# Kernel tuning notes

Hardware: AMD Instinct MI355X
Metric: run time of the kernel (lower is better)

Reference implementation:

```python
import jax, jax.numpy as jnp
import numpy as np

B, T, D, H = 2, 2048, 1024, 16
DH = D // H

def setup_inputs() -> dict:
    key = jax.random.key(0)
    ks = jax.random.split(key, 5)
    scale = 1.0 / np.sqrt(D)
    x = jax.random.normal(ks[0], (B, T, D), dtype=jnp.float32)
    Wq = jax.random.normal(ks[1], (D, D), dtype=jnp.float32) * scale
    Wk = jax.random.normal(ks[2], (D, D), dtype=jnp.float32) * scale
    Wv = jax.random.normal(ks[3], (D, D), dtype=jnp.float32) * scale
    Wo = jax.random.normal(ks[4], (D, D), dtype=jnp.float32) * scale
    # causal mask: True means masked (matches torch masked_fill semantics)
    mask = jnp.triu(jnp.ones((T, T), dtype=bool), k=1)
    return {"x": x, "mask": mask, "Wq": Wq, "Wk": Wk, "Wv": Wv, "Wo": Wo}

def reference(x, mask, Wq, Wk, Wv, Wo):
    b, t, c = x.shape
    # projections -> [B, H, T, DH]
    def split_heads(y):
        return y.reshape(b, t, H, DH).transpose(0, 2, 1, 3)
    q = split_heads(x @ Wq)
    k = split_heads(x @ Wk)
    v = split_heads(x @ Wv)
    # scores [B, H, T, T]
    att = jnp.einsum('bhqd,bhkd->bhqk', q, k) / jnp.sqrt(jnp.float32(DH))
    att = jnp.where(mask, -jnp.inf, att)
    att = jax.nn.softmax(att, axis=-1)
    # dropout=0.0 (eval-mode determinism)
    out = jnp.einsum('bhqk,bhkd->bhqd', att, v)
    out = out.transpose(0, 2, 1, 3).reshape(b, t, c)
    return out @ Wo
```

## Files before the change

kernel.cpp:

```cpp
#include <hip/hip_runtime.h>
#include <stdint.h>

typedef unsigned short u16;
typedef unsigned int u32;
typedef __attribute__((ext_vector_type(8))) short s16x8;
typedef __attribute__((ext_vector_type(4))) float f32x4;
typedef __attribute__((ext_vector_type(8))) unsigned short u16x8;
typedef __attribute__((ext_vector_type(4))) unsigned short u16x4;

#define T_ 2048
#define D_ 1024
#define H_ 16
#define DH_ 64

#define QSCALE_LOG2E 0.18033688011112042f

#if __has_builtin(__builtin_amdgcn_exp2f)
#define EXP2(x) __builtin_amdgcn_exp2f(x)
#else
#define EXP2(x) exp2f(x)
#endif

__device__ __forceinline__ float bf2f(u16 u) {
    union { unsigned int i; float f; } x; x.i = ((unsigned int)u) << 16; return x.f;
}
__device__ __forceinline__ u16 f2bf(float f) {
    union { float f; unsigned int i; } x; x.f = f;
    unsigned int u = x.i;
    u += 0x7fffu + ((u >> 16) & 1u);
    return (u16)(u >> 16);
}
__device__ __forceinline__ u32 pack_rn(float a, float b) {
    union { float f; u32 u; } ua, ub; ua.f = a; ub.f = b;
    return ((ua.u + 0x8000u) >> 16) | ((ub.u + 0x8000u) & 0xffff0000u);
}
__device__ __forceinline__ u32 cvtpk(float lo, float hi) {
    u32 r;
    asm("v_cvt_pk_bf16_f32 %0, %1, %2" : "=v"(r) : "v"(lo), "v"(hi));
    return r;
}
__device__ __forceinline__ void plswap32(u32 &a, u32 &b) {
    asm("v_permlane32_swap_b32 %0, %1" : "+v"(a), "+v"(b));
}
__device__ __forceinline__ void plswap16(u32 &a, u32 &b) {
    asm("v_permlane16_swap_b32 %0, %1" : "+v"(a), "+v"(b));
}
__device__ __forceinline__ s16x8 frag4(u32 a, u32 b, u32 c, u32 d) {
    union { u32 u[4]; s16x8 v; } x;
    x.u[0] = a; x.u[1] = b; x.u[2] = c; x.u[3] = d; return x.v;
}
__device__ __forceinline__ void p_frags(const f32x4 s[4], s16x8 &p0, s16x8 &p1) {
    u32 w00 = cvtpk(s[0][0], s[0][1]), w01 = cvtpk(s[0][2], s[0][3]);
    u32 w10 = cvtpk(s[1][0], s[1][1]), w11 = cvtpk(s[1][2], s[1][3]);
    u32 w20 = cvtpk(s[2][0], s[2][1]), w21 = cvtpk(s[2][2], s[2][3]);
    u32 w30 = cvtpk(s[3][0], s[3][1]), w31 = cvtpk(s[3][2], s[3][3]);
    plswap32(w00, w10); plswap16(w00, w10);
    plswap32(w01, w11); plswap16(w01, w11);
    plswap32(w20, w30); plswap16(w20, w30);
    plswap32(w21, w31); plswap16(w21, w31);
    p0 = frag4(w00, w01, w10, w11);
    p1 = frag4(w20, w21, w30, w31);
}

__device__ __forceinline__ void gload16(const u16* g, u16* l) {
    __builtin_amdgcn_global_load_lds(
        (const __attribute__((address_space(1))) void*)g,
        (__attribute__((address_space(3))) void*)l,
        16, 0, 0);
}

__global__ __launch_bounds__(256) void prep_kernel(const float* __restrict__ x,
                                                   const float* __restrict__ Wq,
                                                   const float* __restrict__ Wk,
                                                   const float* __restrict__ Wv,
                                                   const float* __restrict__ Wo,
                                                   u16* __restrict__ xb,
                                                   u16* __restrict__ WT) {
    __shared__ float tile[32][33];
    int blk = blockIdx.x;
    if (blk < 4096) {
        int i = (blk * 256 + threadIdx.x) * 4;
        float4 v = *(const float4*)(x + i);
        u16x4 o;
        o[0] = f2bf(v.x); o[1] = f2bf(v.y); o[2] = f2bf(v.z); o[3] = f2bf(v.w);
        *(u16x4*)(xb + i) = o;
    } else {
        int t = blk - 4096;
        int s = t >> 10;
        const float* W = (s == 0) ? Wq : (s == 1) ? Wk : (s == 2) ? Wv : Wo;
        int n0 = ((t >> 5) & 31) * 32;
        int k0 = (t & 31) * 32;
        int tx = threadIdx.x & 31, ty = threadIdx.x >> 5;
        #pragma unroll
        for (int j = 0; j < 32; j += 8)
            tile[ty + j][tx] = W[(k0 + ty + j) * D_ + n0 + tx];
        __syncthreads();
        u16* dst = WT + (size_t)s * D_ * D_;
        int row = threadIdx.x >> 3;
        int cg  = (threadIdx.x & 7) << 2;
        u16x4 o;
        #pragma unroll
        for (int j = 0; j < 4; ++j) o[j] = f2bf(tile[cg + j][row]);
        *(u16x4*)(dst + (size_t)(n0 + row) * D_ + k0 + cg) = o;
    }
}

__global__ __launch_bounds__(256) void gemm_qkv(const u16* __restrict__ A,
                                                const u16* __restrict__ Bt,
                                                u16* __restrict__ Qw,
                                                u16* __restrict__ Kw,
                                                u16* __restrict__ Vw) {
    __shared__ __align__(16) u16 As[2][128 * 32];
    __shared__ __align__(16) u16 Bs[2][128 * 32];
    const int m0 = blockIdx.x * 128, n0 = blockIdx.y * 128;
    int tid = threadIdx.x;
    int w = tid >> 6, lane = tid & 63, quad = lane >> 4, l15 = lane & 15;
    int wr = w >> 1, wc = w & 1;

    int nb0 = (w << 7), nb1 = nb0 + 64;
    int c0 = nb0 + lane, c1 = nb1 + lane;
    int r0 = c0 >> 2, k0off = (((c0 & 3) ^ ((r0 >> 1) & 3)) << 3);
    int r1 = c1 >> 2, k1off = (((c1 & 3) ^ ((r1 >> 1) & 3)) << 3);
    const u16* Ar0 = A + (size_t)(m0 + r0) * D_ + k0off;
    const u16* Ar1 = A + (size_t)(m0 + r1) * D_ + k1off;
    const u16* Br0 = Bt + (size_t)(n0 + r0) * D_ + k0off;
    const u16* Br1 = Bt + (size_t)(n0 + r1) * D_ + k1off;

    f32x4 acc[4][4];
    #pragma unroll
    for (int mi = 0; mi < 4; ++mi)
        #pragma unroll
        for (int ni = 0; ni < 4; ++ni) acc[mi][ni] = (f32x4){0.f, 0.f, 0.f, 0.f};

    gload16(Ar0, &As[0][nb0 << 3]);
    gload16(Ar1, &As[0][nb1 << 3]);
    gload16(Br0, &Bs[0][nb0 << 3]);
    gload16(Br1, &Bs[0][nb1 << 3]);

    for (int k0 = 0; k0 < D_; k0 += 32) {
        int buf = (k0 >> 5) & 1;
        __syncthreads();
        if (k0 + 32 < D_) {
            int kn = k0 + 32;
            gload16(Ar0 + kn, &As[buf ^ 1][nb0 << 3]);
            gload16(Ar1 + kn, &As[buf ^ 1][nb1 << 3]);
            gload16(Br0 + kn, &Bs[buf ^ 1][nb0 << 3]);
            gload16(Br1 + kn, &Bs[buf ^ 1][nb1 << 3]);
        }
        s16x8 af[4], bf[4];
        #pragma unroll
        for (int mi = 0; mi < 4; ++mi) {
            int R = wr * 64 + mi * 16 + l15;
            af[mi] = *(const s16x8*)&As[buf][((R << 2) | (quad ^ ((R >> 1) & 3))) << 3];
        }
        #pragma unroll
        for (int ni = 0; ni < 4; ++ni) {
            int R = wc * 64 + ni * 16 + l15;
            bf[ni] = *(const s16x8*)&Bs[buf][((R << 2) | (quad ^ ((R >> 1) & 3))) << 3];
        }
        #pragma unroll
        for (int mi = 0; mi < 4; ++mi)
            #pragma unroll
            for (int ni = 0; ni < 4; ++ni)
                acc[mi][ni] = __builtin_amdgcn_mfma_f32_16x16x32_bf16(af[mi], bf[ni],
                                                                      acc[mi][ni], 0, 0, 0);
    }

    #pragma unroll
    for (int mi = 0; mi < 4; ++mi) {
        int mbase = m0 + wr * 64 + mi * 16 + quad * 4;
        #pragma unroll
        for (int ni = 0; ni < 4; ++ni) {
            int n = n0 + wc * 64 + ni * 16 + l15;
            int b = mbase >> 11, t0 = mbase & 2047;
            int sel = n >> 10, nn = n & 1023;
            int h = nn >> 6, dh = nn & 63;
            int bhidx = (b << 4) + h;
            if (sel == 0) {
                #pragma unroll
                for (int r = 0; r < 4; ++r)
                    Qw[(size_t)(bhidx * T_ + t0 + r) * DH_ + dh] =
                        f2bf(acc[mi][ni][r] * QSCALE_LOG2E);
            } else if (sel == 1) {
                #pragma unroll
                for (int r = 0; r < 4; ++r)
                    Kw[(size_t)(bhidx * T_ + t0 + r) * DH_ + dh] = f2bf(acc[mi][ni][r]);
            } else {
                uint2 pk;
                pk.x = pack_rn(acc[mi][ni][0], acc[mi][ni][1]);
                pk.y = pack_rn(acc[mi][ni][2], acc[mi][ni][3]);
                *(uint2*)(Vw + ((size_t)bhidx * DH_ + dh) * T_ + t0) = pk;
            }
        }
    }
}

__global__ __launch_bounds__(256) void gemm_out(const u16* __restrict__ A,
                                                const u16* __restrict__ Bt,
                                                float* __restrict__ Cout) {
    __shared__ __align__(16) u16 As[2][128 * 32];
    __shared__ __align__(16) u16 Bs[2][128 * 32];
    const int m0 = blockIdx.x * 128, n0 = blockIdx.y * 128;
    int tid = threadIdx.x;
    int w = tid >> 6, lane = tid & 63, quad = lane >> 4, l15 = lane & 15;
    int wr = w >> 1, wc = w & 1;

    int nb0 = (w << 7), nb1 = nb0 + 64;
    int c0 = nb0 + lane, c1 = nb1 + lane;
    int r0 = c0 >> 2, k0off = (((c0 & 3) ^ ((r0 >> 1) & 3)) << 3);
    int r1 = c1 >> 2, k1off = (((c1 & 3) ^ ((r1 >> 1) & 3)) << 3);
    const u16* Ar0 = A + (size_t)(m0 + r0) * D_ + k0off;
    const u16* Ar1 = A + (size_t)(m0 + r1) * D_ + k1off;
    const u16* Br0 = Bt + (size_t)(n0 + r0) * D_ + k0off;
    const u16* Br1 = Bt + (size_t)(n0 + r1) * D_ + k1off;

    f32x4 acc[4][4];
    #pragma unroll
    for (int mi = 0; mi < 4; ++mi)
        #pragma unroll
        for (int ni = 0; ni < 4; ++ni) acc[mi][ni] = (f32x4){0.f, 0.f, 0.f, 0.f};

    gload16(Ar0, &As[0][nb0 << 3]);
    gload16(Ar1, &As[0][nb1 << 3]);
    gload16(Br0, &Bs[0][nb0 << 3]);
    gload16(Br1, &Bs[0][nb1 << 3]);

    for (int k0 = 0; k0 < D_; k0 += 32) {
        int buf = (k0 >> 5) & 1;
        __syncthreads();
        if (k0 + 32 < D_) {
            int kn = k0 + 32;
            gload16(Ar0 + kn, &As[buf ^ 1][nb0 << 3]);
            gload16(Ar1 + kn, &As[buf ^ 1][nb1 << 3]);
            gload16(Br0 + kn, &Bs[buf ^ 1][nb0 << 3]);
            gload16(Br1 + kn, &Bs[buf ^ 1][nb1 << 3]);
        }
        s16x8 af[4], bf[4];
        #pragma unroll
        for (int mi = 0; mi < 4; ++mi) {
            int R = wr * 64 + mi * 16 + l15;
            af[mi] = *(const s16x8*)&As[buf][((R << 2) | (quad ^ ((R >> 1) & 3))) << 3];
        }
        #pragma unroll
        for (int ni = 0; ni < 4; ++ni) {
            int R = wc * 64 + ni * 16 + l15;
            bf[ni] = *(const s16x8*)&Bs[buf][((R << 2) | (quad ^ ((R >> 1) & 3))) << 3];
        }
        #pragma unroll
        for (int mi = 0; mi < 4; ++mi)
            #pragma unroll
            for (int ni = 0; ni < 4; ++ni)
                acc[mi][ni] = __builtin_amdgcn_mfma_f32_16x16x32_bf16(af[mi], bf[ni],
                                                                      acc[mi][ni], 0, 0, 0);
    }

    #pragma unroll
    for (int mi = 0; mi < 4; ++mi) {
        int mbase = m0 + wr * 64 + mi * 16 + quad * 4;
        #pragma unroll
        for (int ni = 0; ni < 4; ++ni) {
            int n = n0 + wc * 64 + ni * 16 + l15;
            #pragma unroll
            for (int r = 0; r < 4; ++r)
                Cout[(size_t)(mbase + r) * D_ + n] = acc[mi][ni][r];
        }
    }
}

__global__ __launch_bounds__(256, 4) void attn_mfma_kernel(const u16* __restrict__ Qg,
                                                           const u16* __restrict__ Kg,
                                                           const u16* __restrict__ Vt,
                                                           u16* __restrict__ Opart,
                                                           float* __restrict__ lpart) {
    __shared__ __align__(16) u16 Kbuf[2][64 * 64];
    __shared__ __align__(16) u16 Vbuf[2][64 * 64];

    int blk = blockIdx.x;
    int xcd = blk & 7, slot = blk >> 3;
    int bh = (xcd << 2) + (slot / 40);
    int x  = slot % 40;
    int BX, c;
    if (x < 4)       { BX = x;                    c = 0; }
    else if (x < 12) { BX = 4 + ((x - 4) >> 1);   c = (x - 4) & 1; }
    else if (x < 24) { BX = 8 + (x - 12) / 3;     c = (x - 12) % 3; }
    else             { BX = 12 + ((x - 24) >> 2); c = (x - 24) & 3; }
    int ktm = 2 * BX + 1;
    int ntile = ktm + 1;
    int nch = (BX >> 2) + 1;
    int base = ntile / nch, rem = ntile % nch;
    int kstart = c * base + (c < rem ? c : rem);
    int kend = kstart + base + (c < rem ? 1 : 0);

    int tid = threadIdx.x;
    int w = tid >> 6, lane = tid & 63, quad = lane >> 4, l15 = lane & 15;
    int q0 = BX << 7;
    int qA = q0 + 16 * w;
    int qB = q0 + 64 + 16 * w;

    const u16* Qb = Qg + (size_t)bh * T_ * DH_;
    const u16* Kb = Kg + (size_t)bh * T_ * DH_;
    const u16* Vb = Vt + (size_t)bh * DH_ * T_;

    s16x8 qa0 = *(const s16x8*)(Qb + (size_t)(qA + l15) * DH_ + quad * 8);
    s16x8 qa1 = *(const s16x8*)(Qb + (size_t)(qA + l15) * DH_ + quad * 8 + 32);
    s16x8 qc0 = *(const s16x8*)(Qb + (size_t)(qB + l15) * DH_ + quad * 8);
    s16x8 qc1 = *(const s16x8*)(Qb + (size_t)(qB + l15) * DH_ + quad * 8 + 32);

    const s16x8 ones = frag4(0x3F803F80u, 0x3F803F80u, 0x3F803F80u, 0x3F803F80u);

    int nb0 = (w << 7), nb1 = nb0 + 64;
    int n0c = nb0 + lane, n1c = nb1 + lane;
    int r0 = n0c >> 3, c0s = n0c & 7, g0 = (r0 << 3) + (c0s ^ (r0 & 7));
    int r1 = n1c >> 3, c1s = n1c & 7, g1 = (r1 << 3) + (c1s ^ (r1 & 7));

    {
        int kb0 = kstart << 6;
        const u16* Ktile = Kb + (size_t)kb0 * DH_;
        gload16(Ktile + (g0 << 3), &Kbuf[0][nb0 << 3]);
        gload16(Ktile + (g1 << 3), &Kbuf[0][nb1 << 3]);
        gload16(Vb + (size_t)r0 * T_ + kb0 + ((g0 & 7) << 3), &Vbuf[0][nb0 << 3]);
        gload16(Vb + (size_t)r1 * T_ + kb0 + ((g1 & 7) << 3), &Vbuf[0][nb1 << 3]);
    }

    f32x4 oA[4] = {{0.f,0.f,0.f,0.f},{0.f,0.f,0.f,0.f},{0.f,0.f,0.f,0.f},{0.f,0.f,0.f,0.f}};
    f32x4 oB[4] = {{0.f,0.f,0.f,0.f},{0.f,0.f,0.f,0.f},{0.f,0.f,0.f,0.f},{0.f,0.f,0.f,0.f}};
    f32x4 oLA = {0.f, 0.f, 0.f, 0.f};
    f32x4 oLB = {0.f, 0.f, 0.f, 0.f};

    for (int kt = kstart; kt < kend; ++kt) {
        int buf = (kt - kstart) & 1;
        __syncthreads();

        if (kt + 1 < kend) {
            int kb2 = (kt + 1) << 6;
            const u16* Ktile = Kb + (size_t)kb2 * DH_;
            gload16(Ktile + (g0 << 3), &Kbuf[buf ^ 1][nb0 << 3]);
            gload16(Ktile + (g1 << 3), &Kbuf[buf ^ 1][nb1 << 3]);
            gload16(Vb + (size_t)r0 * T_ + kb2 + ((g0 & 7) << 3), &Vbuf[buf ^ 1][nb0 << 3]);
            gload16(Vb + (size_t)r1 * T_ + kb2 + ((g1 & 7) << 3), &Vbuf[buf ^ 1][nb1 << 3]);
        }

        const bool liveA = (kt < ktm);

        f32x4 sA[4], sB[4];
        #pragma unroll
        for (int g = 0; g < 4; ++g) {
            int r = (g << 4) + l15;
            int cc = quad ^ (r & 7);
            s16x8 ka0 = *(const s16x8*)&Kbuf[buf][((r << 3) + cc) << 3];
            s16x8 ka1 = *(const s16x8*)&Kbuf[buf][((r << 3) + (cc ^ 4)) << 3];
            f32x4 z = {0.f, 0.f, 0.f, 0.f};
            sB[g] = __builtin_amdgcn_mfma_f32_16x16x32_bf16(ka0, qc0, z, 0, 0, 0);
            sB[g] = __builtin_amdgcn_mfma_f32_16x16x32_bf16(ka1, qc1, sB[g], 0, 0, 0);
            if (liveA) {
                sA[g] = __builtin_amdgcn_mfma_f32_16x16x32_bf16(ka0, qa0, z, 0, 0, 0);
                sA[g] = __builtin_amdgcn_mfma_f32_16x16x32_bf16(ka1, qa1, sA[g], 0, 0, 0);
            }
        }

        if (liveA && kt == ktm - 1) {
            int rA = 16 * w + l15;
            #pragma unroll
            for (int g = 0; g < 4; ++g)
                #pragma unroll
                for (int r = 0; r < 4; ++r)
                    if ((g << 4) + (quad << 2) + r > rA) sA[g][r] = -INFINITY;
        }
        if (kt == ktm) {
            int rB = 16 * w + l15;
            #pragma unroll
            for (int g = 0; g < 4; ++g)
                #pragma unroll
                for (int r = 0; r < 4; ++r)
                    if ((g << 4) + (quad << 2) + r > rB) sB[g][r] = -INFINITY;
        }

        #pragma unroll
        for (int g = 0; g < 4; ++g) {
            sB[g][0] = EXP2(sB[g][0]);
            sB[g][1] = EXP2(sB[g][1]);
            sB[g][2] = EXP2(sB[g][2]);
            sB[g][3] = EXP2(sB[g][3]);
        }
        if (liveA) {
            #pragma unroll
            for (int g = 0; g < 4; ++g) {
                sA[g][0] = EXP2(sA[g][0]);
                sA[g][1] = EXP2(sA[g][1]);
                sA[g][2] = EXP2(sA[g][2]);
                sA[g][3] = EXP2(sA[g][3]);
            }
        }

        s16x8 pa0, pa1, pc0, pc1;
        p_frags(sB, pc0, pc1);
        if (liveA) p_frags(sA, pa0, pa1);

        oLB = __builtin_amdgcn_mfma_f32_16x16x32_bf16(ones, pc0, oLB, 0, 0, 0);
        oLB = __builtin_amdgcn_mfma_f32_16x16x32_bf16(ones, pc1, oLB, 0, 0, 0);
        if (liveA) {
            oLA = __builtin_amdgcn_mfma_f32_16x16x32_bf16(ones, pa0, oLA, 0, 0, 0);
            oLA = __builtin_amdgcn_mfma_f32_16x16x32_bf16(ones, pa1, oLA, 0, 0, 0);
        }

        #pragma unroll
        for (int g = 0; g < 4; ++g) {
            int r = (g << 4) + l15;
            int cc = quad ^ (r & 7);
            s16x8 va0 = *(const s16x8*)&Vbuf[buf][((r << 3) + cc) << 3];
            s16x8 va1 = *(const s16x8*)&Vbuf[buf][((r << 3) + (cc ^ 4)) << 3];
            oB[g] = __builtin_amdgcn_mfma_f32_16x16x32_bf16(va0, pc0, oB[g], 0, 0, 0);
            oB[g] = __builtin_amdgcn_mfma_f32_16x16x32_bf16(va1, pc1, oB[g], 0, 0, 0);
            if (liveA) {
                oA[g] = __builtin_amdgcn_mfma_f32_16x16x32_bf16(va0, pa0, oA[g], 0, 0, 0);
                oA[g] = __builtin_amdgcn_mfma_f32_16x16x32_bf16(va1, pa1, oA[g], 0, 0, 0);
            }
        }
    }

    int slotid = ((bh << 4) + BX) * 4 + c;
    u16* dA = Opart + ((size_t)slotid * 128 + 16 * w + l15) * 64;
    u16* dB = dA + 64 * 64;
    #pragma unroll
    for (int g = 0; g < 4; ++g) {
        uint2 pk;
        pk.x = cvtpk(oA[g][0], oA[g][1]); pk.y = cvtpk(oA[g][2], oA[g][3]);
        *(uint2*)(dA + (g << 4) + (quad << 2)) = pk;
        pk.x = cvtpk(oB[g][0], oB[g][1]); pk.y = cvtpk(oB[g][2], oB[g][3]);
        *(uint2*)(dB + (g << 4) + (quad << 2)) = pk;
    }
    if (quad == 0) {
        lpart[(size_t)slotid * 128 + 16 * w + l15] = oLA[0];
        lpart[(size_t)slotid * 128 + 64 + 16 * w + l15] = oLB[0];
    }
}

__global__ __launch_bounds__(256) void reduce_attn(const u16* __restrict__ Opart,
                                                   const float* __restrict__ lpart,
                                                   u16* __restrict__ att) {
    int BX = blockIdx.x, bh = blockIdx.y;
    int nch = (BX >> 2) + 1;
    int tid = threadIdx.x;
    int row = tid >> 1, dh0 = (tid & 1) << 5;
    int slotbase = ((bh << 4) + BX) << 2;

    float acc[32];
    #pragma unroll
    for (int i = 0; i < 32; ++i) acc[i] = 0.f;
    float l = 0.f;
    for (int cc = 0; cc < nch; ++cc) {
        const u16* op = Opart + ((size_t)(slotbase + cc) * 128 + row) * 64 + dh0;
        #pragma unroll
        for (int v = 0; v < 4; ++v) {
            u16x8 o8 = *(const u16x8*)(op + v * 8);
            #pragma unroll
            for (int j = 0; j < 8; ++j) acc[v * 8 + j] += bf2f(o8[j]);
        }
        l += lpart[(size_t)(slotbase + cc) * 128 + row];
    }
    float inv = 1.f / l;
    int b = bh >> 4, h = bh & 15;
    int q = (BX << 7) + row;
    u16* dst = att + ((size_t)(b * T_) + q) * D_ + (h << 6) + dh0;
    #pragma unroll
    for (int v = 0; v < 4; ++v) {
        u16x8 o8;
        #pragma unroll
        for (int j = 0; j < 8; ++j) o8[j] = f2bf(acc[v * 8 + j] * inv);
        *(u16x8*)(dst + v * 8) = o8;
    }
}

extern "C" void kernel_launch(void* const* d_in, const int* in_sizes, int n_in,
                              void* d_out, int out_size, void* d_ws, size_t ws_size,
                              hipStream_t stream) {
    const float* x  = (const float*)d_in[0];
    const float* Wq = (const float*)d_in[2];
    const float* Wk = (const float*)d_in[3];
    const float* Wv = (const float*)d_in[4];
    const float* Wo = (const float*)d_in[5];
    float* out = (float*)d_out;

    char* ws = (char*)d_ws;
    u16*   xb    = (u16*)(ws);
    u16*   WT    = (u16*)(ws + (8ull  << 20));
    u16*   Qw    = (u16*)(ws + (16ull << 20));
    u16*   Kw    = (u16*)(ws + (24ull << 20));
    u16*   Vw    = (u16*)(ws + (32ull << 20));
    u16*   att   = (u16*)(ws + (40ull << 20));
    u16*   Opart = (u16*)(ws + (48ull << 20));
    float* lpart = (float*)(ws + (82ull << 20));

    prep_kernel<<<dim3(8192), dim3(256), 0, stream>>>(x, Wq, Wk, Wv, Wo, xb, WT);
    gemm_qkv<<<dim3(32, 24), dim3(256), 0, stream>>>(xb, WT, Qw, Kw, Vw);
    attn_mfma_kernel<<<dim3(1280), dim3(256), 0, stream>>>(Qw, Kw, Vw, Opart, lpart);
    reduce_attn<<<dim3(16, 32), dim3(256), 0, stream>>>(Opart, lpart, att);
    gemm_out<<<dim3(32, 8), dim3(256), 0, stream>>>(att, WT + 3ull * 1048576ull, out);
}
```

Measured before the change: 186.3 us.

## Write unsplit attention tiles directly and halve output GEMM tile width

Attention tiles that run as a single KV chunk (nch==1) now normalise by the row sum and write bf16 output straight into the attention buffer. This skips the partial-buffer round trip, and reduce_attn now launches only for the split tiles (BX>=4). Separately, gemm_out switches from 128x128 to 128x64 tiles, doubling the grid to 512 blocks to improve CU occupancy on the small output GEMM, at the cost of more redundant A-tile loads.

```diff
diff --git a/kernel.cpp b/kernel.cpp
--- a/kernel.cpp
+++ b/kernel.cpp
@@ -199,55 +199,52 @@
                                                 const u16* __restrict__ Bt,
                                                 float* __restrict__ Cout) {
     __shared__ __align__(16) u16 As[2][128 * 32];
-    __shared__ __align__(16) u16 Bs[2][128 * 32];
-    const int m0 = blockIdx.x * 128, n0 = blockIdx.y * 128;
+    __shared__ __align__(16) u16 Bs[2][64 * 32];
+    const int m0 = blockIdx.x * 128, n0 = blockIdx.y * 64;
     int tid = threadIdx.x;
     int w = tid >> 6, lane = tid & 63, quad = lane >> 4, l15 = lane & 15;
-    int wr = w >> 1, wc = w & 1;
-
-    int nb0 = (w << 7), nb1 = nb0 + 64;
-    int c0 = nb0 + lane, c1 = nb1 + lane;
-    int r0 = c0 >> 2, k0off = (((c0 & 3) ^ ((r0 >> 1) & 3)) << 3);
-    int r1 = c1 >> 2, k1off = (((c1 & 3) ^ ((r1 >> 1) & 3)) << 3);
-    const u16* Ar0 = A + (size_t)(m0 + r0) * D_ + k0off;
-    const u16* Ar1 = A + (size_t)(m0 + r1) * D_ + k1off;
-    const u16* Br0 = Bt + (size_t)(n0 + r0) * D_ + k0off;
-    const u16* Br1 = Bt + (size_t)(n0 + r1) * D_ + k1off;
-
-    f32x4 acc[4][4];
+
+    int nbA0 = (w << 7), nbA1 = nbA0 + 64, nbB = (w << 6);
+    int cA0 = nbA0 + lane, cA1 = nbA1 + lane, cB = nbB + lane;
+    int rA0 = cA0 >> 2, kA0 = (((cA0 & 3) ^ ((rA0 >> 1) & 3)) << 3);
+    int rA1 = cA1 >> 2, kA1 = (((cA1 & 3) ^ ((rA1 >> 1) & 3)) << 3);
+    int rB  = cB >> 2,  kB  = (((cB  & 3) ^ ((rB  >> 1) & 3)) << 3);
+    const u16* ArA0 = A + (size_t)(m0 + rA0) * D_ + kA0;
+    const u16* ArA1 = A + (size_t)(m0 + rA1) * D_ + kA1;
+    const u16* BrB  = Bt + (size_t)(n0 + rB) * D_ + kB;
+
+    f32x4 acc[2][4];
     #pragma unroll
-    for (int mi = 0; mi < 4; ++mi)
+    for (int mi = 0; mi < 2; ++mi)
         #pragma unroll
         for (int ni = 0; ni < 4; ++ni) acc[mi][ni] = (f32x4){0.f, 0.f, 0.f, 0.f};
 
-    gload16(Ar0, &As[0][nb0 << 3]);
-    gload16(Ar1, &As[0][nb1 << 3]);
-    gload16(Br0, &Bs[0][nb0 << 3]);
-    gload16(Br1, &Bs[0][nb1 << 3]);
+    gload16(ArA0, &As[0][nbA0 << 3]);
+    gload16(ArA1, &As[0][nbA1 << 3]);
+    gload16(BrB,  &Bs[0][nbB << 3]);
 
     for (int k0 = 0; k0 < D_; k0 += 32) {
         int buf = (k0 >> 5) & 1;
         __syncthreads();
         if (k0 + 32 < D_) {
             int kn = k0 + 32;
-            gload16(Ar0 + kn, &As[buf ^ 1][nb0 << 3]);
-            gload16(Ar1 + kn, &As[buf ^ 1][nb1 << 3]);
-            gload16(Br0 + kn, &Bs[buf ^ 1][nb0 << 3]);
-            gload16(Br1 + kn, &Bs[buf ^ 1][nb1 << 3]);
-        }
-        s16x8 af[4], bf[4];
-        #pragma unroll
-        for (int mi = 0; mi < 4; ++mi) {
-            int R = wr * 64 + mi * 16 + l15;
+            gload16(ArA0 + kn, &As[buf ^ 1][nbA0 << 3]);
+            gload16(ArA1 + kn, &As[buf ^ 1][nbA1 << 3]);
+            gload16(BrB + kn,  &Bs[buf ^ 1][nbB << 3]);
+        }
+        s16x8 af[2], bf[4];
+        #pragma unroll
+        for (int mi = 0; mi < 2; ++mi) {
+            int R = w * 32 + mi * 16 + l15;
             af[mi] = *(const s16x8*)&As[buf][((R << 2) | (quad ^ ((R >> 1) & 3))) << 3];
         }
         #pragma unroll
         for (int ni = 0; ni < 4; ++ni) {
-            int R = wc * 64 + ni * 16 + l15;
+            int R = ni * 16 + l15;
             bf[ni] = *(const s16x8*)&Bs[buf][((R << 2) | (quad ^ ((R >> 1) & 3))) << 3];
         }
         #pragma unroll
-        for (int mi = 0; mi < 4; ++mi)
+        for (int mi = 0; mi < 2; ++mi)
             #pragma unroll
             for (int ni = 0; ni < 4; ++ni)
                 acc[mi][ni] = __builtin_amdgcn_mfma_f32_16x16x32_bf16(af[mi], bf[ni],
@@ -255,11 +252,11 @@
     }
 
     #pragma unroll
-    for (int mi = 0; mi < 4; ++mi) {
-        int mbase = m0 + wr * 64 + mi * 16 + quad * 4;
+    for (int mi = 0; mi < 2; ++mi) {
+        int mbase = m0 + w * 32 + mi * 16 + quad * 4;
         #pragma unroll
         for (int ni = 0; ni < 4; ++ni) {
-            int n = n0 + wc * 64 + ni * 16 + l15;
+            int n = n0 + ni * 16 + l15;
             #pragma unroll
             for (int r = 0; r < 4; ++r)
                 Cout[(size_t)(mbase + r) * D_ + n] = acc[mi][ni][r];
@@ -271,7 +268,8 @@
                                                            const u16* __restrict__ Kg,
                                                            const u16* __restrict__ Vt,
                                                            u16* __restrict__ Opart,
-                                                           float* __restrict__ lpart) {
+                                                           float* __restrict__ lpart,
+                                                           u16* __restrict__ att) {
     __shared__ __align__(16) u16 Kbuf[2][64 * 64];
     __shared__ __align__(16) u16 Vbuf[2][64 * 64];
 
@@ -418,27 +416,45 @@
         }
     }
 
-    int slotid = ((bh << 4) + BX) * 4 + c;
-    u16* dA = Opart + ((size_t)slotid * 128 + 16 * w + l15) * 64;
-    u16* dB = dA + 64 * 64;
-    #pragma unroll
-    for (int g = 0; g < 4; ++g) {
-        uint2 pk;
-        pk.x = cvtpk(oA[g][0], oA[g][1]); pk.y = cvtpk(oA[g][2], oA[g][3]);
-        *(uint2*)(dA + (g << 4) + (quad << 2)) = pk;
-        pk.x = cvtpk(oB[g][0], oB[g][1]); pk.y = cvtpk(oB[g][2], oB[g][3]);
-        *(uint2*)(dB + (g << 4) + (quad << 2)) = pk;
-    }
-    if (quad == 0) {
-        lpart[(size_t)slotid * 128 + 16 * w + l15] = oLA[0];
-        lpart[(size_t)slotid * 128 + 64 + 16 * w + l15] = oLB[0];
+    if (nch == 1) {
+        float iA = 1.f / oLA[0];
+        float iB = 1.f / oLB[0];
+        int b = bh >> 4, h = bh & 15;
+        u16* da = att + ((size_t)(b * T_ + q0 + 16 * w + l15)) * D_ + (h << 6);
+        u16* db = att + ((size_t)(b * T_ + q0 + 64 + 16 * w + l15)) * D_ + (h << 6);
+        #pragma unroll
+        for (int g = 0; g < 4; ++g) {
+            uint2 pk;
+            pk.x = cvtpk(oA[g][0] * iA, oA[g][1] * iA);
+            pk.y = cvtpk(oA[g][2] * iA, oA[g][3] * iA);
+            *(uint2*)(da + (g << 4) + (quad << 2)) = pk;
+            pk.x = cvtpk(oB[g][0] * iB, oB[g][1] * iB);
+            pk.y = cvtpk(oB[g][2] * iB, oB[g][3] * iB);
+            *(uint2*)(db + (g << 4) + (quad << 2)) = pk;
+        }
+    } else {
+        int slotid = ((bh << 4) + BX) * 4 + c;
+        u16* dA = Opart + ((size_t)slotid * 128 + 16 * w + l15) * 64;
+        u16* dB = dA + 64 * 64;
+        #pragma unroll
+        for (int g = 0; g < 4; ++g) {
+            uint2 pk;
+            pk.x = cvtpk(oA[g][0], oA[g][1]); pk.y = cvtpk(oA[g][2], oA[g][3]);
+            *(uint2*)(dA + (g << 4) + (quad << 2)) = pk;
+            pk.x = cvtpk(oB[g][0], oB[g][1]); pk.y = cvtpk(oB[g][2], oB[g][3]);
+            *(uint2*)(dB + (g << 4) + (quad << 2)) = pk;
+        }
+        if (quad == 0) {
+            lpart[(size_t)slotid * 128 + 16 * w + l15] = oLA[0];
+            lpart[(size_t)slotid * 128 + 64 + 16 * w + l15] = oLB[0];
+        }
     }
 }
 
 __global__ __launch_bounds__(256) void reduce_attn(const u16* __restrict__ Opart,
                                                    const float* __restrict__ lpart,
                                                    u16* __restrict__ att) {
-    int BX = blockIdx.x, bh = blockIdx.y;
+    int BX = blockIdx.x + 4, bh = blockIdx.y;
     int nch = (BX >> 2) + 1;
     int tid = threadIdx.x;
     int row = tid >> 1, dh0 = (tid & 1) << 5;
@@ -493,7 +509,7 @@
 
     prep_kernel<<<dim3(8192), dim3(256), 0, stream>>>(x, Wq, Wk, Wv, Wo, xb, WT);
     gemm_qkv<<<dim3(32, 24), dim3(256), 0, stream>>>(xb, WT, Qw, Kw, Vw);
-    attn_mfma_kernel<<<dim3(1280), dim3(256), 0, stream>>>(Qw, Kw, Vw, Opart, lpart);
-    reduce_attn<<<dim3(16, 32), dim3(256), 0, stream>>>(Opart, lpart, att);
-    gemm_out<<<dim3(32, 8), dim3(256), 0, stream>>>(att, WT + 3ull * 1048576ull, out);
-}
+    attn_mfma_kernel<<<dim3(1280), dim3(256), 0, stream>>>(Qw, Kw, Vw, Opart, lpart, att);
+    reduce_attn<<<dim3(12, 32), dim3(256), 0, stream>>>(Opart, lpart, att);
+    gemm_out<<<dim3(32, 16), dim3(256), 0, stream>>>(att, WT + 3ull * 1048576ull, out);
+}
```

Measured after the change: 187.5 us. Within noise of the previous version (+0.6%).
